# Optimization experiments

Hardware: AMD Instinct MI355X
Metric: run time of the kernel (lower is better)

## Reference

```python
import jax, jax.numpy as jnp
import numpy as np

B, G = 256, 24
N = B * G
D_IN, HEADS, D_HEAD = 128, 8, 64  # out_channels = in_channels//2 = 64, concat=False
EFF = HEADS * D_HEAD
EPS = 1e-5
SCALE = float(np.sqrt(D_HEAD))

def _gelu(x):
    return jax.nn.gelu(x, approximate=False)

def _pff(x, w1, b1, w2, b2):
    # PositionwiseFeedForward, dropout=0 (eval)
    return _gelu(x @ w1.T + b1) @ w2.T + b2

def _graph_norm_global(x, w, b, ms):
    # GraphNorm called without batch -> single graph over all N nodes
    mean = jnp.mean(x, axis=0, keepdims=True)
    out = x - mean * ms
    var = jnp.mean(out * out, axis=0, keepdims=True)
    return w * out / jnp.sqrt(var + EPS) + b

def _graph_norm(x, w, b, ms, batch, nseg):
    cnt = jax.ops.segment_sum(jnp.ones((x.shape[0],), x.dtype), batch, nseg)[:, None]
    mean = jax.ops.segment_sum(x, batch, nseg) / cnt
    out = x - mean[batch] * ms
    var = jax.ops.segment_sum(out * out, batch, nseg) / cnt
    return w * out / jnp.sqrt(var + EPS)[batch] + b

def _segment_softmax(logits, seg, nseg):
    m = jax.ops.segment_max(logits, seg, num_segments=nseg)
    e = jnp.exp(logits - m[seg])
    s = jax.ops.segment_sum(e, seg, num_segments=nseg)
    return e / (s[seg] + 1e-16)

def _attn_conv(x, edge_index, p):
    (nq_w, nq_b, nq_ms, wq, bq, wk, bk, wv, bv,
     no_w, no_b, no_ms, o_w1, o_b1, o_w2, o_b2) = p
    n = x.shape[0]
    xin = x
    xn = _graph_norm_global(x, nq_w, nq_b, nq_ms)
    q = (xn @ wq.T + bq).reshape(n, HEADS, D_HEAD)
    k = (xn @ wk.T + bk).reshape(n, HEADS, D_HEAD)
    v = (xn @ wv.T + bv).reshape(n, HEADS, D_HEAD)
    loops = jnp.arange(n, dtype=edge_index.dtype)  # add_self_loops appends
    src = jnp.concatenate([edge_index[0], loops])
    dst = jnp.concatenate([edge_index[1], loops])
    qk = jnp.sum(q[dst] * k[src], axis=-1) / SCALE          # [E', H]
    alpha = _segment_softmax(qk, dst, n)                     # segment softmax over dst
    aggr = jax.ops.segment_sum(v[src] * alpha[:, :, None], dst, num_segments=n)  # [N,H,Dh]
    aggr = aggr.mean(axis=1)                                 # concat=False: head mean -> [N,64]
    init = xin.reshape(n, D_IN // D_HEAD, D_HEAD).sum(axis=1)  # sum-fold 128 -> 64 residual
    h = aggr + init
    hn = _graph_norm_global(h, no_w, no_b, no_ms)
    return h + _pff(hn, o_w1, o_b1, o_w2, o_b2)


def setup_inputs() -> dict:
    key = jax.random.key(0)
    ks = jax.random.split(key, 12)
    # block-dense edges: fully connected within each set, no self loops
    a = np.arange(G)
    ii, jj = np.meshgrid(a, a, indexing='ij')
    m = ii != jj
    dst_l, src_l = ii[m], jj[m]
    offs = (np.arange(B) * G)[:, None]
    src = (src_l[None, :] + offs).reshape(-1)
    dst = (dst_l[None, :] + offs).reshape(-1)
    edge_index = jnp.asarray(np.stack([src, dst]), dtype=jnp.int64)
    batch = jnp.asarray(np.repeat(np.arange(B), G), dtype=jnp.int64)
    ptr = jnp.asarray(np.arange(B + 1) * G, dtype=jnp.int64)
    x = jax.random.normal(ks[0], (N, D_IN), jnp.float32)
    def lin(k, o, i):
        return jax.random.normal(k, (o, i), jnp.float32) * (1.0 / np.sqrt(i))
    d = dict(x=x, edge_index=edge_index, ptr=ptr, batch=batch)
    d.update(nq_w=jnp.ones((D_IN,)), nq_b=jnp.zeros((D_IN,)), nq_ms=jnp.ones((D_IN,)))
    d.update(wq=lin(ks[1], EFF, D_IN), bq=jnp.zeros((EFF,)),
             wk=lin(ks[2], EFF, D_IN), bk=jnp.zeros((EFF,)),
             wv=lin(ks[3], EFF, D_IN), bv=jnp.zeros((EFF,)))
    d.update(no_w=jnp.ones((D_HEAD,)), no_b=jnp.zeros((D_HEAD,)), no_ms=jnp.ones((D_HEAD,)))
    d.update(o_w1=lin(ks[4], D_HEAD, D_HEAD), o_b1=jnp.zeros((D_HEAD,)),
             o_w2=lin(ks[5], D_HEAD, D_HEAD), o_b2=jnp.zeros((D_HEAD,)))
    d.update(pn_w=jnp.ones((D_HEAD,)), pn_b=jnp.zeros((D_HEAD,)), pn_ms=jnp.ones((D_HEAD,)))
    d.update(p_w1=lin(ks[6], D_HEAD, D_HEAD), p_b1=jnp.zeros((D_HEAD,)),
             p_w2=lin(ks[7], 1, D_HEAD), p_b2=jnp.zeros((1,)))
    return d


def reference(x, edge_index, ptr, batch,
              nq_w, nq_b, nq_ms, wq, bq, wk, bk, wv, bv,
              no_w, no_b, no_ms, o_w1, o_b1, o_w2, o_b2,
              pn_w, pn_b, pn_ms, p_w1, p_b1, p_w2, p_b2):
    nseg = ptr.shape[0] - 1
    h = _attn_conv(x, edge_index,
                   (nq_w, nq_b, nq_ms, wq, bq, wk, bk, wv, bv,
                    no_w, no_b, no_ms, o_w1, o_b1, o_w2, o_b2))   # [N,64]
    hn = _graph_norm(h, pn_w, pn_b, pn_ms, batch, nseg)
    score = _pff(hn, p_w1, p_b1, p_w2, p_b2)                       # [N,1]
    w = _segment_softmax(score[:, 0], batch, nseg)[:, None]        # per-set softmax
    return jax.ops.segment_sum(x * w, batch, num_segments=nseg)    # [B, 128]
```

## Files before the change

kernel.cpp:

```cpp
#include <hip/hip_runtime.h>
#include <stdint.h>


#define N_NODES 6144
#define GSIZE 24
#define NGRAPH 256
#define DIN 128
#define DH 64
#define EFF 512
#define EPSN 1e-5f

typedef __attribute__((ext_vector_type(8))) __bf16 bf16x8;
typedef __attribute__((ext_vector_type(4))) float f32x4;
union U16B { uint4 u; bf16x8 v; unsigned short s[8]; };

__device__ inline float bf2f(unsigned short u){ return __uint_as_float(((unsigned)u)<<16); }
__device__ inline unsigned short f2bf(float f){
  unsigned u = __float_as_uint(f);
  u += 0x7fff + ((u>>16)&1);
  return (unsigned short)(u>>16);
}
__device__ inline float gelu_exact(float x){ return 0.5f*x*(1.0f+erff(x*0.70710678118654752f)); }

#define XP    0
#define HP    49152
#define WT1   81920
#define WT2   86016
#define PWT1  90112
#define FBo   94208
#define WCVT_BYTE  385024
#define HCOMB_BYTE 778240

__global__ __launch_bounds__(256)
void k_pre(const float* __restrict__ x,
           const float* __restrict__ o_w1, const float* __restrict__ o_w2,
           const float* __restrict__ p_w1,
           const float* __restrict__ o_b1, const float* __restrict__ o_b2,
           const float* __restrict__ p_b1, const float* __restrict__ p_w2,
           const float* __restrict__ p_b2,
           const float* __restrict__ wq, const float* __restrict__ wk,
           const float* __restrict__ wv,
           float* __restrict__ wsf){
  int t = threadIdx.x;
  int bi = blockIdx.x;
  if(bi < 192){
    int c = t & 127, h = t >> 7;
    float s = 0.f, q = 0.f;
    #pragma unroll
    for(int r = 0; r < 16; ++r){
      float v = x[(size_t)(bi*32 + h + 2*r)*DIN + c];
      s += v; q += v*v;
    }
    __shared__ float sm[256], sm2[256];
    sm[t] = s; sm2[t] = q;
    __syncthreads();
    if(t < 128){
      wsf[XP + bi*256 + t]       = sm[t] + sm[t+128];
      wsf[XP + bi*256 + 128 + t] = sm2[t] + sm2[t+128];
    }
    return;
  }
  if(bi < 195){
    const float* src; float* dst;
    if(bi == 192){ src = o_w1; dst = wsf + WT1; }
    else if(bi == 193){ src = o_w2; dst = wsf + WT2; }
    else { src = p_w1; dst = wsf + PWT1; }
    for(int p = t; p < DH*DH; p += 256){
      int r = p >> 6, c = p & 63;
      dst[c*DH + r] = src[p];
    }
    if(bi == 192){
      float* fb = wsf + FBo;
      if(t < 64){
        fb[t]       = o_b1[t];
        fb[64 + t]  = o_b2[t];
        fb[128 + t] = p_b1[t];
        fb[192 + t] = p_w2[t];
      }
      if(t == 0) fb[256] = p_b2[0];
    }
    return;
  }
  int j = bi - 195;
  int mat = j >> 2, seg = j & 3;
  const float* src = (mat==0) ? wq : (mat==1) ? wk : wv;
  unsigned short* dst = (unsigned short*)((char*)wsf + WCVT_BYTE)
                        + (size_t)mat*EFF*DIN + seg*16384;
  const float* sp = src + seg*16384;
  for(int e = t*8; e < 16384; e += 2048){
    float4 a = *(const float4*)(sp + e);
    float4 b = *(const float4*)(sp + e + 4);
    U16B o;
    o.s[0]=f2bf(a.x); o.s[1]=f2bf(a.y); o.s[2]=f2bf(a.z); o.s[3]=f2bf(a.w);
    o.s[4]=f2bf(b.x); o.s[5]=f2bf(b.y); o.s[6]=f2bf(b.z); o.s[7]=f2bf(b.w);
    *(uint4*)(dst + e) = o.u;
  }
}

__global__ __launch_bounds__(512, 1)
void k_fused(const float* __restrict__ x,
             const float* __restrict__ bq, const float* __restrict__ bk,
             const float* __restrict__ bv,
             const float* __restrict__ nq_w, const float* __restrict__ nq_b,
             const float* __restrict__ nq_ms,
             float* __restrict__ ws, float* __restrict__ hcomb){
  __shared__ __align__(16) char arena[52224];
  float (*hv)[68] = (float(*)[68])(arena);
  float* A1 = (float*)(arena + 6528);
  float* C1 = (float*)(arena + 7040);
  float (*qs)[GSIZE][68] = (float(*)[GSIZE][68])(arena + 7552);
  float (*ks)[GSIZE][68] = (float(*)[GSIZE][68])(arena + 20608);
  float (*vs)[GSIZE][68] = (float(*)[GSIZE][68])(arena + 33664);
  float (*S)[GSIZE][28]  = (float(*)[GSIZE][28])(arena + 46720);
  float* redA = (float*)(arena + 7552);
  float* redB = (float*)(arena + 11648);

  int t = threadIdx.x, g = blockIdx.x, base = g * GSIZE;
  const unsigned short* wcvt = (const unsigned short*)((const char*)ws + WCVT_BYTE);

  {
    int c = t & 127, grp = t >> 7;
    float s = 0.f, q = 0.f;
    for(int p = grp*48; p < grp*48 + 48; ++p){
      s += ws[XP + p*256 + c];
      q += ws[XP + p*256 + 128 + c];
    }
    redA[t] = s; redB[t] = q;
  }
  __syncthreads();
  if(t < 128){
    float s = redA[t] + redA[t+128] + redA[t+256] + redA[t+384];
    float q = redB[t] + redB[t+128] + redB[t+256] + redB[t+384];
    float mean = s * (1.0f / N_NODES);
    float ex2  = q * (1.0f / N_NODES);
    float cm   = mean * nq_ms[t];
    float var  = ex2 - 2.f*cm*mean + cm*cm;
    float rstd = rsqrtf(var + EPSN);
    float a    = nq_w[t] * rstd;
    A1[t] = a; C1[t] = nq_b[t] - a*cm;
  }
  __syncthreads();

  int pipe = t >> 8, t2 = t & 255;
  int wv4 = (t >> 6) & 3, lane = t & 63, m = lane & 15, quad = lane >> 4;
  int mt = wv4 & 1, cth = wv4 >> 1;
  int node = mt*16 + m;
  int xrow = base + node; if(xrow > N_NODES-1) xrow = N_NODES-1;

  bf16x8 xfr[4];
  #pragma unroll
  for(int kk = 0; kk < 4; kk++){
    int k0 = kk*32 + quad*8;
    float4 a = *(const float4*)(x + (size_t)xrow*DIN + k0);
    float4 b = *(const float4*)(x + (size_t)xrow*DIN + k0 + 4);
    U16B u;
    u.s[0] = f2bf(a.x*A1[k0+0] + C1[k0+0]);
    u.s[1] = f2bf(a.y*A1[k0+1] + C1[k0+1]);
    u.s[2] = f2bf(a.z*A1[k0+2] + C1[k0+2]);
    u.s[3] = f2bf(a.w*A1[k0+3] + C1[k0+3]);
    u.s[4] = f2bf(b.x*A1[k0+4] + C1[k0+4]);
    u.s[5] = f2bf(b.y*A1[k0+5] + C1[k0+5]);
    u.s[6] = f2bf(b.z*A1[k0+6] + C1[k0+6]);
    u.s[7] = f2bf(b.w*A1[k0+7] + C1[k0+7]);
    xfr[kk] = u.v;
  }

  uint4 wbuf[6][4];
  float4 bb[6];
  {
    int hh = pipe;
    #pragma unroll
    for(int task = 0; task < 6; ++task){
      int tk = cth*6 + task;
      int mat = tk >> 2, ctm = tk & 3;
      const unsigned short* wp = wcvt + (size_t)mat*EFF*DIN
                               + (size_t)(hh*64 + ctm*16 + m)*DIN + quad*8;
      #pragma unroll
      for(int kk = 0; kk < 4; kk++) wbuf[task][kk] = *(const uint4*)(wp + kk*32);
      const float* bias = (mat==0) ? bq : (mat==1) ? bk : bv;
      bb[task] = *(const float4*)(bias + hh*64 + ctm*16 + quad*4);
    }
  }

  f32x4 a0 = {0.f,0.f,0.f,0.f}, a1 = {0.f,0.f,0.f,0.f};

  for(int iter = 0; iter < 4; ++iter){
    __syncthreads();
    #pragma unroll
    for(int task = 0; task < 6; ++task){
      int tk = cth*6 + task;
      int mat = tk >> 2, ctm = tk & 3;
      f32x4 acc = {0.f,0.f,0.f,0.f};
      #pragma unroll
      for(int kk = 0; kk < 4; kk++){
        U16B w8; w8.u = wbuf[task][kk];
        acc = __builtin_amdgcn_mfma_f32_16x16x32_bf16(w8.v, xfr[kk], acc, 0, 0, 0);
      }
      float (*tile)[68] = (mat==0) ? qs[pipe] : (mat==1) ? ks[pipe] : vs[pipe];
      if(mt == 0 || m < 8){
        int d0 = ctm*16 + quad*4;
        tile[node][d0+0] = acc[0] + bb[task].x;
        tile[node][d0+1] = acc[1] + bb[task].y;
        tile[node][d0+2] = acc[2] + bb[task].z;
        tile[node][d0+3] = acc[3] + bb[task].w;
      }
    }
    __syncthreads();
    if(iter < 3){
      int hh = (iter+1)*2 + pipe;
      #pragma unroll
      for(int task = 0; task < 6; ++task){
        int tk = cth*6 + task;
        int mat = tk >> 2, ctm = tk & 3;
        const unsigned short* wp = wcvt + (size_t)mat*EFF*DIN
                                 + (size_t)(hh*64 + ctm*16 + m)*DIN + quad*8;
        #pragma unroll
        for(int kk = 0; kk < 4; kk++) wbuf[task][kk] = *(const uint4*)(wp + kk*32);
        const float* bias = (mat==0) ? bq : (mat==1) ? bk : bv;
        bb[task] = *(const float4*)(bias + hh*64 + ctm*16 + quad*4);
      }
    }
    if(t2 < 192){
      int row = t2 >> 3, sl = t2 & 7;
      const float4* qi = (const float4*)qs[pipe][row];
      const float4* k0p = (const float4*)ks[pipe][sl*3];
      const float4* k1p = (const float4*)ks[pipe][sl*3+1];
      const float4* k2p = (const float4*)ks[pipe][sl*3+2];
      float s0 = 0.f, s1 = 0.f, s2 = 0.f;
      #pragma unroll
      for(int d = 0; d < 16; ++d){
        float4 qv = qi[d];
        float4 ka = k0p[d], kb = k1p[d], kc = k2p[d];
        s0 += qv.x*ka.x + qv.y*ka.y + qv.z*ka.z + qv.w*ka.w;
        s1 += qv.x*kb.x + qv.y*kb.y + qv.z*kb.z + qv.w*kb.w;
        s2 += qv.x*kc.x + qv.y*kc.y + qv.z*kc.z + qv.w*kc.w;
      }
      s0 *= 0.125f; s1 *= 0.125f; s2 *= 0.125f;
      float m0 = fmaxf(fmaxf(s0, s1), s2);
      #pragma unroll
      for(int o = 1; o < 8; o <<= 1) m0 = fmaxf(m0, __shfl_xor(m0, o, 8));
      float e0 = __expf(s0-m0), e1 = __expf(s1-m0), e2 = __expf(s2-m0);
      float su = e0 + e1 + e2;
      #pragma unroll
      for(int o = 1; o < 8; o <<= 1) su += __shfl_xor(su, o, 8);
      float inv = 1.0f / (su + 1e-16f);
      S[pipe][row][sl*3]   = e0*inv;
      S[pipe][row][sl*3+1] = e1*inv;
      S[pipe][row][sl*3+2] = e2*inv;
    }
    __syncthreads();
    {
      int p = t2;
      if(p < 384){
        int i = p >> 4, dq = p & 15;
        #pragma unroll 8
        for(int j = 0; j < GSIZE; ++j){
          float w = S[pipe][i][j];
          float4 v = *(const float4*)&vs[pipe][j][dq*4];
          a0.x += w*v.x; a0.y += w*v.y; a0.z += w*v.z; a0.w += w*v.w;
        }
      }
      p = t2 + 256;
      if(p < 384){
        int i = p >> 4, dq = p & 15;
        #pragma unroll 8
        for(int j = 0; j < GSIZE; ++j){
          float w = S[pipe][i][j];
          float4 v = *(const float4*)&vs[pipe][j][dq*4];
          a1.x += w*v.x; a1.y += w*v.y; a1.z += w*v.z; a1.w += w*v.w;
        }
      }
    }
  }
  __syncthreads();
  if(pipe == 1){
    int p = t2;
    if(p < 384){
      int i = p >> 4, dq = p & 15;
      float4 o; o.x = a0.x*0.125f; o.y = a0.y*0.125f; o.z = a0.z*0.125f; o.w = a0.w*0.125f;
      *(float4*)&hv[i][dq*4] = o;
    }
    p = t2 + 256;
    if(p < 384){
      int i = p >> 4, dq = p & 15;
      float4 o; o.x = a1.x*0.125f; o.y = a1.y*0.125f; o.z = a1.z*0.125f; o.w = a1.w*0.125f;
      *(float4*)&hv[i][dq*4] = o;
    }
  }
  __syncthreads();
  if(pipe == 0){
    #pragma unroll
    for(int slot = 0; slot < 2; ++slot){
      int p = t2 + slot*256;
      if(p < 384){
        int i = p >> 4, dq = p & 15;
        f32x4 a = slot ? a1 : a0;
        float4 hp = *(const float4*)&hv[i][dq*4];
        const float* xr = x + (size_t)(base+i)*DIN + dq*4;
        float4 r1 = *(const float4*)xr;
        float4 r2 = *(const float4*)(xr + 64);
        float4 o;
        o.x = a.x*0.125f + hp.x + r1.x + r2.x;
        o.y = a.y*0.125f + hp.y + r1.y + r2.y;
        o.z = a.z*0.125f + hp.z + r1.z + r2.z;
        o.w = a.w*0.125f + hp.w + r1.w + r2.w;
        *(float4*)&hv[i][dq*4] = o;
        *(float4*)(hcomb + (size_t)(base+i)*DH + dq*4) = o;
      }
    }
  }
  __syncthreads();
  if(t < 64){
    float s1 = 0.f, s2 = 0.f;
    #pragma unroll
    for(int i = 0; i < GSIZE; ++i){ float v = hv[i][t]; s1 += v; s2 += v*v; }
    ws[HP + g*128 + t]      = s1;
    ws[HP + g*128 + 64 + t] = s2;
  }
}

__global__ __launch_bounds__(256)
void k_final(const float* __restrict__ x,
             const float* __restrict__ hbuf, const float* __restrict__ ws,
             const float* __restrict__ no_w, const float* __restrict__ no_b,
             const float* __restrict__ no_ms,
             const float* __restrict__ pn_w, const float* __restrict__ pn_b,
             const float* __restrict__ pn_ms,
             float* __restrict__ out){
  const float* wt1  = ws + WT1;
  const float* wt2  = ws + WT2;
  const float* pwt1 = ws + PWT1;
  const float* fb   = ws + FBo;

  __shared__ float hs[GSIZE][DH+1];
  __shared__ float hn[GSIZE][DH+1];
  __shared__ float ts[GSIZE][DH+1];
  __shared__ float A2[DH], C2[DH];
  __shared__ float a3[DH], c3[DH];
  __shared__ float scores[GSIZE], wsm[GSIZE];
  __shared__ float redA[256], redB[256];

  int t = threadIdx.x;
  int base = blockIdx.x * GSIZE;

  {
    int c = t & 63, grp = t >> 6;
    float s1 = 0.f, s2 = 0.f;
    for(int p = grp; p < NGRAPH; p += 4){
      s1 += ws[HP + p*128 + c];
      s2 += ws[HP + p*128 + 64 + c];
    }
    redA[t] = s1; redB[t] = s2;
  }
  __syncthreads();
  if(t < DH){
    float s1 = redA[t] + redA[t+64] + redA[t+128] + redA[t+192];
    float s2 = redB[t] + redB[t+64] + redB[t+128] + redB[t+192];
    float mean = s1 * (1.0f / N_NODES);
    float ex2  = s2 * (1.0f / N_NODES);
    float cm   = mean * no_ms[t];
    float var  = ex2 - 2.f*cm*mean + cm*cm;
    float rstd = rsqrtf(var + EPSN);
    float a    = no_w[t] * rstd;
    A2[t] = a; C2[t] = no_b[t] - a*cm;
  }
  __syncthreads();
  for(int p = t; p < GSIZE*DH; p += 256){
    int i = p >> 6, d = p & 63;
    float hvv = hbuf[(size_t)(base+i)*DH + d];
    hs[i][d] = hvv;
    hn[i][d] = A2[d]*hvv + C2[d];
  }
  __syncthreads();
  for(int p = t; p < GSIZE*DH; p += 256){
    int i = p >> 6, c = p & 63;
    float s = fb[c];
    #pragma unroll
    for(int k = 0; k < DH; k++) s += hn[i][k] * wt1[k*DH + c];
    ts[i][c] = gelu_exact(s);
  }
  __syncthreads();
  for(int p = t; p < GSIZE*DH; p += 256){
    int i = p >> 6, c = p & 63;
    float s = fb[64 + c];
    #pragma unroll
    for(int k = 0; k < DH; k++) s += ts[i][k] * wt2[k*DH + c];
    hs[i][c] = hs[i][c] + s;
  }
  __syncthreads();
  if(t < DH){
    float s1 = 0.f, s2 = 0.f;
    for(int i = 0; i < GSIZE; i++){ float v = hs[i][t]; s1 += v; s2 += v*v; }
    float mean = s1 * (1.0f / GSIZE);
    float ex2  = s2 * (1.0f / GSIZE);
    float cm   = mean * pn_ms[t];
    float var  = ex2 - 2.f*cm*mean + cm*cm;
    float rstd = rsqrtf(var + EPSN);
    float a    = pn_w[t] * rstd;
    a3[t] = a; c3[t] = pn_b[t] - a*cm;
  }
  __syncthreads();
  for(int p = t; p < GSIZE*DH; p += 256){
    int i = p >> 6, d = p & 63;
    hn[i][d] = a3[d]*hs[i][d] + c3[d];
  }
  __syncthreads();
  for(int p = t; p < GSIZE*DH; p += 256){
    int i = p >> 6, c = p & 63;
    float s = fb[128 + c];
    #pragma unroll
    for(int k = 0; k < DH; k++) s += hn[i][k] * pwt1[k*DH + c];
    ts[i][c] = gelu_exact(s);
  }
  __syncthreads();
  if(t < GSIZE){
    float s = fb[256];
    for(int c = 0; c < DH; c++) s += ts[t][c] * fb[192 + c];
    scores[t] = s;
  }
  __syncthreads();
  if(t < GSIZE){
    float mx = -1e30f;
    for(int j = 0; j < GSIZE; j++) mx = fmaxf(mx, scores[j]);
    float sum = 0.f;
    for(int j = 0; j < GSIZE; j++) sum += __expf(scores[j] - mx);
    wsm[t] = __expf(scores[t] - mx) / (sum + 1e-16f);
  }
  __syncthreads();
  if(t < DIN){
    float s = 0.f;
    #pragma unroll 8
    for(int i = 0; i < GSIZE; i++) s += wsm[i] * x[(size_t)(base+i)*DIN + t];
    out[(size_t)blockIdx.x*DIN + t] = s;
  }
}

extern "C" void kernel_launch(void* const* d_in, const int* in_sizes, int n_in,
                              void* d_out, int out_size, void* d_ws, size_t ws_size,
                              hipStream_t stream){
  (void)in_sizes; (void)n_in; (void)out_size; (void)ws_size;
  const float* x    = (const float*)d_in[0];
  const float* nq_w = (const float*)d_in[4];
  const float* nq_b = (const float*)d_in[5];
  const float* nq_ms= (const float*)d_in[6];
  const float* wq   = (const float*)d_in[7];
  const float* bq   = (const float*)d_in[8];
  const float* wk   = (const float*)d_in[9];
  const float* bk   = (const float*)d_in[10];
  const float* wv   = (const float*)d_in[11];
  const float* bv   = (const float*)d_in[12];
  const float* no_w = (const float*)d_in[13];
  const float* no_b = (const float*)d_in[14];
  const float* no_ms= (const float*)d_in[15];
  const float* o_w1 = (const float*)d_in[16];
  const float* o_b1 = (const float*)d_in[17];
  const float* o_w2 = (const float*)d_in[18];
  const float* o_b2 = (const float*)d_in[19];
  const float* pn_w = (const float*)d_in[20];
  const float* pn_b = (const float*)d_in[21];
  const float* pn_ms= (const float*)d_in[22];
  const float* p_w1 = (const float*)d_in[23];
  const float* p_b1 = (const float*)d_in[24];
  const float* p_w2 = (const float*)d_in[25];
  const float* p_b2 = (const float*)d_in[26];

  float* ws = (float*)d_ws;
  float* hcomb = (float*)((char*)d_ws + HCOMB_BYTE);

  k_pre<<<207, 256, 0, stream>>>(x, o_w1, o_w2, p_w1, o_b1, o_b2, p_b1, p_w2, p_b2,
                                 wq, wk, wv, ws);
  k_fused<<<NGRAPH, 512, 0, stream>>>(x, bq, bk, bv, nq_w, nq_b, nq_ms, ws, hcomb);
  k_final<<<NGRAPH, 256, 0, stream>>>(x, hcomb, ws, no_w, no_b, no_ms,
                                      pn_w, pn_b, pn_ms, (float*)d_out);
}
```

Measured before the change: 182.2 us.

## Split per-graph attention across four blocks with atomic last-block reduction

The fused attention kernel now launches 1024 blocks of 256 threads, each handling two heads of one graph, instead of 256 blocks of 512 threads handling all eight heads. Partial head sums go to a workspace buffer, and the last block per graph, found through an atomic counter, reduces them. The global-norm statistics are finalized once in the pre-kernel by a last-block pattern rather than redundantly in every block. The final kernel also stages the two 64x64 FFN weights in shared memory. The cost is an extra memset, atomics, and partial-sum traffic through global memory.

```diff
diff --git a/kernel.cpp b/kernel.cpp
--- a/kernel.cpp
+++ b/kernel.cpp
@@ -22,14 +22,18 @@
 }
 __device__ inline float gelu_exact(float x){ return 0.5f*x*(1.0f+erff(x*0.70710678118654752f)); }
 
-#define XP    0
-#define HP    49152
-#define WT1   81920
-#define WT2   86016
-#define PWT1  90112
-#define FBo   94208
-#define WCVT_BYTE  385024
-#define HCOMB_BYTE 778240
+#define XP     0
+#define A1C1   49152
+#define HP     49408
+#define WT1    82176
+#define WT2    86272
+#define PWT1   90368
+#define FBo    94464
+#define XPCNT  95232
+#define CNT    95233
+#define WCVT_BYTE  382976
+#define HPART_BYTE 776192
+#define HCOMB_BYTE 7067648
 
 __global__ __launch_bounds__(256)
 void k_pre(const float* __restrict__ x,
@@ -40,6 +44,8 @@
            const float* __restrict__ p_b2,
            const float* __restrict__ wq, const float* __restrict__ wk,
            const float* __restrict__ wv,
+           const float* __restrict__ nq_w, const float* __restrict__ nq_b,
+           const float* __restrict__ nq_ms,
            float* __restrict__ wsf){
   int t = threadIdx.x;
   int bi = blockIdx.x;
@@ -52,11 +58,35 @@
       s += v; q += v*v;
     }
     __shared__ float sm[256], sm2[256];
+    __shared__ int lastf;
     sm[t] = s; sm2[t] = q;
     __syncthreads();
     if(t < 128){
       wsf[XP + bi*256 + t]       = sm[t] + sm[t+128];
       wsf[XP + bi*256 + 128 + t] = sm2[t] + sm2[t+128];
+    }
+    __syncthreads();
+    if(t == 0){
+      __threadfence();
+      int old = atomicAdd((int*)(wsf + XPCNT), 1);
+      lastf = (old == 191);
+    }
+    __syncthreads();
+    if(!lastf) return;
+    __threadfence();
+    float acc = 0.f;
+    for(int p = 0; p < 192; ++p) acc += wsf[XP + p*256 + t];
+    sm[t] = acc;
+    __syncthreads();
+    if(t < 128){
+      float mean = sm[t] * (1.0f / N_NODES);
+      float ex2  = sm[128+t] * (1.0f / N_NODES);
+      float cm   = mean * nq_ms[t];
+      float var  = ex2 - 2.f*cm*mean + cm*cm;
+      float rstd = rsqrtf(var + EPSN);
+      float a    = nq_w[t] * rstd;
+      wsf[A1C1 + t]       = a;
+      wsf[A1C1 + 128 + t] = nq_b[t] - a*cm;
     }
     return;
   }
@@ -97,78 +127,52 @@
   }
 }
 
-__global__ __launch_bounds__(512, 1)
+__global__ __launch_bounds__(256, 4)
 void k_fused(const float* __restrict__ x,
              const float* __restrict__ bq, const float* __restrict__ bk,
              const float* __restrict__ bv,
-             const float* __restrict__ nq_w, const float* __restrict__ nq_b,
-             const float* __restrict__ nq_ms,
              float* __restrict__ ws, float* __restrict__ hcomb){
-  __shared__ __align__(16) char arena[52224];
-  float (*hv)[68] = (float(*)[68])(arena);
-  float* A1 = (float*)(arena + 6528);
-  float* C1 = (float*)(arena + 7040);
-  float (*qs)[GSIZE][68] = (float(*)[GSIZE][68])(arena + 7552);
-  float (*ks)[GSIZE][68] = (float(*)[GSIZE][68])(arena + 20608);
-  float (*vs)[GSIZE][68] = (float(*)[GSIZE][68])(arena + 33664);
-  float (*S)[GSIZE][28]  = (float(*)[GSIZE][28])(arena + 46720);
-  float* redA = (float*)(arena + 7552);
-  float* redB = (float*)(arena + 11648);
-
-  int t = threadIdx.x, g = blockIdx.x, base = g * GSIZE;
+  __shared__ __align__(16) float hv[GSIZE][68];
+  __shared__ float A1s[128], C1s[128];
+  __shared__ __align__(16) float qs[GSIZE][68], ks[GSIZE][68], vs[GSIZE][68];
+  __shared__ __align__(16) float S[GSIZE][28];
+  __shared__ int lastf;
+
+  int t = threadIdx.x, b = blockIdx.x;
+  int g = b >> 2, quarter = b & 3, base = g * GSIZE;
   const unsigned short* wcvt = (const unsigned short*)((const char*)ws + WCVT_BYTE);
-
-  {
-    int c = t & 127, grp = t >> 7;
-    float s = 0.f, q = 0.f;
-    for(int p = grp*48; p < grp*48 + 48; ++p){
-      s += ws[XP + p*256 + c];
-      q += ws[XP + p*256 + 128 + c];
-    }
-    redA[t] = s; redB[t] = q;
-  }
-  __syncthreads();
-  if(t < 128){
-    float s = redA[t] + redA[t+128] + redA[t+256] + redA[t+384];
-    float q = redB[t] + redB[t+128] + redB[t+256] + redB[t+384];
-    float mean = s * (1.0f / N_NODES);
-    float ex2  = q * (1.0f / N_NODES);
-    float cm   = mean * nq_ms[t];
-    float var  = ex2 - 2.f*cm*mean + cm*cm;
-    float rstd = rsqrtf(var + EPSN);
-    float a    = nq_w[t] * rstd;
-    A1[t] = a; C1[t] = nq_b[t] - a*cm;
-  }
-  __syncthreads();
-
-  int pipe = t >> 8, t2 = t & 255;
-  int wv4 = (t >> 6) & 3, lane = t & 63, m = lane & 15, quad = lane >> 4;
+  float* hpart = (float*)((char*)ws + HPART_BYTE);
+
+  if(t < 128){ A1s[t] = ws[A1C1 + t]; C1s[t] = ws[A1C1 + 128 + t]; }
+  __syncthreads();
+
+  int wv4 = t >> 6, lane = t & 63, m = lane & 15, quad = lane >> 4;
   int mt = wv4 & 1, cth = wv4 >> 1;
   int node = mt*16 + m;
-  int xrow = base + node; if(xrow > N_NODES-1) xrow = N_NODES-1;
+  int xrow = base + ((node < GSIZE) ? node : 0);
 
   bf16x8 xfr[4];
   #pragma unroll
   for(int kk = 0; kk < 4; kk++){
     int k0 = kk*32 + quad*8;
     float4 a = *(const float4*)(x + (size_t)xrow*DIN + k0);
-    float4 b = *(const float4*)(x + (size_t)xrow*DIN + k0 + 4);
+    float4 bfl = *(const float4*)(x + (size_t)xrow*DIN + k0 + 4);
     U16B u;
-    u.s[0] = f2bf(a.x*A1[k0+0] + C1[k0+0]);
-    u.s[1] = f2bf(a.y*A1[k0+1] + C1[k0+1]);
-    u.s[2] = f2bf(a.z*A1[k0+2] + C1[k0+2]);
-    u.s[3] = f2bf(a.w*A1[k0+3] + C1[k0+3]);
-    u.s[4] = f2bf(b.x*A1[k0+4] + C1[k0+4]);
-    u.s[5] = f2bf(b.y*A1[k0+5] + C1[k0+5]);
-    u.s[6] = f2bf(b.z*A1[k0+6] + C1[k0+6]);
-    u.s[7] = f2bf(b.w*A1[k0+7] + C1[k0+7]);
+    u.s[0] = f2bf(a.x*A1s[k0+0] + C1s[k0+0]);
+    u.s[1] = f2bf(a.y*A1s[k0+1] + C1s[k0+1]);
+    u.s[2] = f2bf(a.z*A1s[k0+2] + C1s[k0+2]);
+    u.s[3] = f2bf(a.w*A1s[k0+3] + C1s[k0+3]);
+    u.s[4] = f2bf(bfl.x*A1s[k0+4] + C1s[k0+4]);
+    u.s[5] = f2bf(bfl.y*A1s[k0+5] + C1s[k0+5]);
+    u.s[6] = f2bf(bfl.z*A1s[k0+6] + C1s[k0+6]);
+    u.s[7] = f2bf(bfl.w*A1s[k0+7] + C1s[k0+7]);
     xfr[kk] = u.v;
   }
 
   uint4 wbuf[6][4];
   float4 bb[6];
   {
-    int hh = pipe;
+    int hh = quarter*2;
     #pragma unroll
     for(int task = 0; task < 6; ++task){
       int tk = cth*6 + task;
@@ -184,7 +188,7 @@
 
   f32x4 a0 = {0.f,0.f,0.f,0.f}, a1 = {0.f,0.f,0.f,0.f};
 
-  for(int iter = 0; iter < 4; ++iter){
+  for(int iter = 0; iter < 2; ++iter){
     __syncthreads();
     #pragma unroll
     for(int task = 0; task < 6; ++task){
@@ -196,7 +200,7 @@
         U16B w8; w8.u = wbuf[task][kk];
         acc = __builtin_amdgcn_mfma_f32_16x16x32_bf16(w8.v, xfr[kk], acc, 0, 0, 0);
       }
-      float (*tile)[68] = (mat==0) ? qs[pipe] : (mat==1) ? ks[pipe] : vs[pipe];
+      float (*tile)[68] = (mat==0) ? qs : (mat==1) ? ks : vs;
       if(mt == 0 || m < 8){
         int d0 = ctm*16 + quad*4;
         tile[node][d0+0] = acc[0] + bb[task].x;
@@ -206,8 +210,8 @@
       }
     }
     __syncthreads();
-    if(iter < 3){
-      int hh = (iter+1)*2 + pipe;
+    if(iter == 0){
+      int hh = quarter*2 + 1;
       #pragma unroll
       for(int task = 0; task < 6; ++task){
         int tk = cth*6 + task;
@@ -220,12 +224,12 @@
         bb[task] = *(const float4*)(bias + hh*64 + ctm*16 + quad*4);
       }
     }
-    if(t2 < 192){
-      int row = t2 >> 3, sl = t2 & 7;
-      const float4* qi = (const float4*)qs[pipe][row];
-      const float4* k0p = (const float4*)ks[pipe][sl*3];
-      const float4* k1p = (const float4*)ks[pipe][sl*3+1];
-      const float4* k2p = (const float4*)ks[pipe][sl*3+2];
+    if(t < 192){
+      int row = t >> 3, sl = t & 7;
+      const float4* qi = (const float4*)qs[row];
+      const float4* k0p = (const float4*)ks[sl*3];
+      const float4* k1p = (const float4*)ks[sl*3+1];
+      const float4* k2p = (const float4*)ks[sl*3+2];
       float s0 = 0.f, s1 = 0.f, s2 = 0.f;
       #pragma unroll
       for(int d = 0; d < 16; ++d){
@@ -244,69 +248,87 @@
       #pragma unroll
       for(int o = 1; o < 8; o <<= 1) su += __shfl_xor(su, o, 8);
       float inv = 1.0f / (su + 1e-16f);
-      S[pipe][row][sl*3]   = e0*inv;
-      S[pipe][row][sl*3+1] = e1*inv;
-      S[pipe][row][sl*3+2] = e2*inv;
+      S[row][sl*3]   = e0*inv;
+      S[row][sl*3+1] = e1*inv;
+      S[row][sl*3+2] = e2*inv;
     }
     __syncthreads();
     {
-      int p = t2;
-      if(p < 384){
-        int i = p >> 4, dq = p & 15;
+      int i = t >> 4, dq = t & 15;
+      #pragma unroll 8
+      for(int j = 0; j < GSIZE; ++j){
+        float w = S[i][j];
+        float4 v = *(const float4*)&vs[j][dq*4];
+        a0.x += w*v.x; a0.y += w*v.y; a0.z += w*v.z; a0.w += w*v.w;
+      }
+      if(t < 128){
+        int p = t + 256; int i2 = p >> 4, dq2 = p & 15;
         #pragma unroll 8
         for(int j = 0; j < GSIZE; ++j){
-          float w = S[pipe][i][j];
-          float4 v = *(const float4*)&vs[pipe][j][dq*4];
-          a0.x += w*v.x; a0.y += w*v.y; a0.z += w*v.z; a0.w += w*v.w;
-        }
-      }
-      p = t2 + 256;
-      if(p < 384){
-        int i = p >> 4, dq = p & 15;
-        #pragma unroll 8
-        for(int j = 0; j < GSIZE; ++j){
-          float w = S[pipe][i][j];
-          float4 v = *(const float4*)&vs[pipe][j][dq*4];
+          float w = S[i2][j];
+          float4 v = *(const float4*)&vs[j][dq2*4];
           a1.x += w*v.x; a1.y += w*v.y; a1.z += w*v.z; a1.w += w*v.w;
         }
       }
     }
   }
   __syncthreads();
-  if(pipe == 1){
-    int p = t2;
-    if(p < 384){
-      int i = p >> 4, dq = p & 15;
-      float4 o; o.x = a0.x*0.125f; o.y = a0.y*0.125f; o.z = a0.z*0.125f; o.w = a0.w*0.125f;
-      *(float4*)&hv[i][dq*4] = o;
-    }
-    p = t2 + 256;
-    if(p < 384){
-      int i = p >> 4, dq = p & 15;
-      float4 o; o.x = a1.x*0.125f; o.y = a1.y*0.125f; o.z = a1.z*0.125f; o.w = a1.w*0.125f;
-      *(float4*)&hv[i][dq*4] = o;
-    }
-  }
-  __syncthreads();
-  if(pipe == 0){
-    #pragma unroll
-    for(int slot = 0; slot < 2; ++slot){
-      int p = t2 + slot*256;
-      if(p < 384){
-        int i = p >> 4, dq = p & 15;
-        f32x4 a = slot ? a1 : a0;
-        float4 hp = *(const float4*)&hv[i][dq*4];
-        const float* xr = x + (size_t)(base+i)*DIN + dq*4;
+  {
+    int i = t >> 4, dq = t & 15;
+    float4 o; o.x = a0.x*0.125f; o.y = a0.y*0.125f; o.z = a0.z*0.125f; o.w = a0.w*0.125f;
+    if(quarter == 0){
+      const float* xr = x + (size_t)(base+i)*DIN + dq*4;
+      float4 r1 = *(const float4*)xr;
+      float4 r2 = *(const float4*)(xr + 64);
+      o.x += r1.x + r2.x; o.y += r1.y + r2.y; o.z += r1.z + r2.z; o.w += r1.w + r2.w;
+    }
+    *(float4*)&hv[i][dq*4] = o;
+    *(float4*)(hpart + ((size_t)b*GSIZE + i)*DH + dq*4) = o;
+    if(t < 128){
+      int p = t + 256; int i2 = p >> 4, dq2 = p & 15;
+      float4 o2; o2.x = a1.x*0.125f; o2.y = a1.y*0.125f; o2.z = a1.z*0.125f; o2.w = a1.w*0.125f;
+      if(quarter == 0){
+        const float* xr = x + (size_t)(base+i2)*DIN + dq2*4;
         float4 r1 = *(const float4*)xr;
         float4 r2 = *(const float4*)(xr + 64);
-        float4 o;
-        o.x = a.x*0.125f + hp.x + r1.x + r2.x;
-        o.y = a.y*0.125f + hp.y + r1.y + r2.y;
-        o.z = a.z*0.125f + hp.z + r1.z + r2.z;
-        o.w = a.w*0.125f + hp.w + r1.w + r2.w;
-        *(float4*)&hv[i][dq*4] = o;
-        *(float4*)(hcomb + (size_t)(base+i)*DH + dq*4) = o;
-      }
+        o2.x += r1.x + r2.x; o2.y += r1.y + r2.y; o2.z += r1.z + r2.z; o2.w += r1.w + r2.w;
+      }
+      *(float4*)&hv[i2][dq2*4] = o2;
+      *(float4*)(hpart + ((size_t)b*GSIZE + i2)*DH + dq2*4) = o2;
+    }
+  }
+  __syncthreads();
+  if(t == 0){
+    __threadfence();
+    int old = atomicAdd((int*)(ws + CNT) + g, 1);
+    lastf = (old == 3);
+  }
+  __syncthreads();
+  if(!lastf) return;
+  __threadfence();
+  {
+    int gb = g << 2;
+    int i = t >> 4, dq = t & 15;
+    float4 o = *(float4*)&hv[i][dq*4];
+    #pragma unroll
+    for(int qq = 0; qq < 4; ++qq){
+      if(qq == quarter) continue;
+      float4 pv = *(const float4*)(hpart + ((size_t)(gb+qq)*GSIZE + i)*DH + dq*4);
+      o.x += pv.x; o.y += pv.y; o.z += pv.z; o.w += pv.w;
+    }
+    *(float4*)&hv[i][dq*4] = o;
+    *(float4*)(hcomb + (size_t)(base+i)*DH + dq*4) = o;
+    if(t < 128){
+      int p = t + 256; int i2 = p >> 4, dq2 = p & 15;
+      float4 o2 = *(float4*)&hv[i2][dq2*4];
+      #pragma unroll
+      for(int qq = 0; qq < 4; ++qq){
+        if(qq == quarter) continue;
+        float4 pv = *(const float4*)(hpart + ((size_t)(gb+qq)*GSIZE + i2)*DH + dq2*4);
+        o2.x += pv.x; o2.y += pv.y; o2.z += pv.z; o2.w += pv.w;
+      }
+      *(float4*)&hv[i2][dq2*4] = o2;
+      *(float4*)(hcomb + (size_t)(base+i2)*DH + dq2*4) = o2;
     }
   }
   __syncthreads();
@@ -327,14 +349,13 @@
              const float* __restrict__ pn_w, const float* __restrict__ pn_b,
              const float* __restrict__ pn_ms,
              float* __restrict__ out){
-  const float* wt1  = ws + WT1;
-  const float* wt2  = ws + WT2;
   const float* pwt1 = ws + PWT1;
   const float* fb   = ws + FBo;
 
-  __shared__ float hs[GSIZE][DH+1];
-  __shared__ float hn[GSIZE][DH+1];
-  __shared__ float ts[GSIZE][DH+1];
+  __shared__ float wt1s[64][64], wt2s[64][64];
+  __shared__ float hs[GSIZE][DH];
+  __shared__ float hn[GSIZE][DH];
+  __shared__ float ts[GSIZE][DH];
   __shared__ float A2[DH], C2[DH];
   __shared__ float a3[DH], c3[DH];
   __shared__ float scores[GSIZE], wsm[GSIZE];
@@ -343,6 +364,10 @@
   int t = threadIdx.x;
   int base = blockIdx.x * GSIZE;
 
+  for(int p = t; p < DH*DH; p += 256){
+    wt1s[p>>6][p&63] = ws[WT1 + p];
+    wt2s[p>>6][p&63] = ws[WT2 + p];
+  }
   {
     int c = t & 63, grp = t >> 6;
     float s1 = 0.f, s2 = 0.f;
@@ -376,7 +401,7 @@
     int i = p >> 6, c = p & 63;
     float s = fb[c];
     #pragma unroll
-    for(int k = 0; k < DH; k++) s += hn[i][k] * wt1[k*DH + c];
+    for(int k = 0; k < DH; k++) s += hn[i][k] * wt1s[k][c];
     ts[i][c] = gelu_exact(s);
   }
   __syncthreads();
@@ -384,7 +409,7 @@
     int i = p >> 6, c = p & 63;
     float s = fb[64 + c];
     #pragma unroll
-    for(int k = 0; k < DH; k++) s += ts[i][k] * wt2[k*DH + c];
+    for(int k = 0; k < DH; k++) s += ts[i][k] * wt2s[k][c];
     hs[i][c] = hs[i][c] + s;
   }
   __syncthreads();
@@ -467,9 +492,10 @@
   float* ws = (float*)d_ws;
   float* hcomb = (float*)((char*)d_ws + HCOMB_BYTE);
 
+  hipMemsetAsync((char*)d_ws + (size_t)XPCNT*4, 0, 1028, stream);
   k_pre<<<207, 256, 0, stream>>>(x, o_w1, o_w2, p_w1, o_b1, o_b2, p_b1, p_w2, p_b2,
-                                 wq, wk, wv, ws);
-  k_fused<<<NGRAPH, 512, 0, stream>>>(x, bq, bk, bv, nq_w, nq_b, nq_ms, ws, hcomb);
+                                 wq, wk, wv, nq_w, nq_b, nq_ms, ws);
+  k_fused<<<1024, 256, 0, stream>>>(x, bq, bk, bv, ws, hcomb);
   k_final<<<NGRAPH, 256, 0, stream>>>(x, hcomb, ws, no_w, no_b, no_ms,
                                       pn_w, pn_b, pn_ms, (float*)d_out);
 }
```

After: 297.0 us. +62.9%, slower.

## Compute input GraphNorm coefficients once in last k_pre block; stage FFN weights in LDS

Applied to the files above, without the earlier changes.

Previously every k_fused block re-reduced all 192 partial column sums to derive the input GraphNorm scale and shift, which is redundant global traffic across 256 blocks. Now the last-arriving k_pre block, detected with an atomic counter and threadfence, computes those coefficients once and stores them in the workspace. k_fused just loads them. k_final also caches the two 64x64 PFF weight matrices in shared memory instead of reading them from global memory in the inner loop. The cost is an extra memset launch to reset the counter, a serialized tail reduction in k_pre, and relaxed launch bounds plus a changed workspace layout.

```diff
diff --git a/kernel.cpp b/kernel.cpp
--- a/kernel.cpp
+++ b/kernel.cpp
@@ -22,14 +22,16 @@
 }
 __device__ inline float gelu_exact(float x){ return 0.5f*x*(1.0f+erff(x*0.70710678118654752f)); }
 
-#define XP    0
-#define HP    49152
-#define WT1   81920
-#define WT2   86016
-#define PWT1  90112
-#define FBo   94208
-#define WCVT_BYTE  385024
-#define HCOMB_BYTE 778240
+#define XP     0
+#define A1C1   49152
+#define HP     49408
+#define WT1    82176
+#define WT2    86272
+#define PWT1   90368
+#define FBo    94464
+#define XPCNT  95232
+#define WCVT_BYTE  382976
+#define HCOMB_BYTE 7067648
 
 __global__ __launch_bounds__(256)
 void k_pre(const float* __restrict__ x,
@@ -40,6 +42,8 @@
            const float* __restrict__ p_b2,
            const float* __restrict__ wq, const float* __restrict__ wk,
            const float* __restrict__ wv,
+           const float* __restrict__ nq_w, const float* __restrict__ nq_b,
+           const float* __restrict__ nq_ms,
            float* __restrict__ wsf){
   int t = threadIdx.x;
   int bi = blockIdx.x;
@@ -52,11 +56,35 @@
       s += v; q += v*v;
     }
     __shared__ float sm[256], sm2[256];
+    __shared__ int lastf;
     sm[t] = s; sm2[t] = q;
     __syncthreads();
     if(t < 128){
       wsf[XP + bi*256 + t]       = sm[t] + sm[t+128];
       wsf[XP + bi*256 + 128 + t] = sm2[t] + sm2[t+128];
+    }
+    __syncthreads();
+    if(t == 0){
+      __threadfence();
+      int old = atomicAdd((int*)(wsf + XPCNT), 1);
+      lastf = (old == 191);
+    }
+    __syncthreads();
+    if(!lastf) return;
+    __threadfence();
+    float acc = 0.f;
+    for(int p = 0; p < 192; ++p) acc += wsf[XP + p*256 + t];
+    sm[t] = acc;
+    __syncthreads();
+    if(t < 128){
+      float mean = sm[t] * (1.0f / N_NODES);
+      float ex2  = sm[128+t] * (1.0f / N_NODES);
+      float cm   = mean * nq_ms[t];
+      float var  = ex2 - 2.f*cm*mean + cm*cm;
+      float rstd = rsqrtf(var + EPSN);
+      float a    = nq_w[t] * rstd;
+      wsf[A1C1 + t]       = a;
+      wsf[A1C1 + 128 + t] = nq_b[t] - a*cm;
     }
     return;
   }
@@ -97,71 +125,43 @@
   }
 }
 
-__global__ __launch_bounds__(512, 1)
+__global__ __launch_bounds__(512)
 void k_fused(const float* __restrict__ x,
              const float* __restrict__ bq, const float* __restrict__ bk,
              const float* __restrict__ bv,
-             const float* __restrict__ nq_w, const float* __restrict__ nq_b,
-             const float* __restrict__ nq_ms,
              float* __restrict__ ws, float* __restrict__ hcomb){
-  __shared__ __align__(16) char arena[52224];
-  float (*hv)[68] = (float(*)[68])(arena);
-  float* A1 = (float*)(arena + 6528);
-  float* C1 = (float*)(arena + 7040);
-  float (*qs)[GSIZE][68] = (float(*)[GSIZE][68])(arena + 7552);
-  float (*ks)[GSIZE][68] = (float(*)[GSIZE][68])(arena + 20608);
-  float (*vs)[GSIZE][68] = (float(*)[GSIZE][68])(arena + 33664);
-  float (*S)[GSIZE][28]  = (float(*)[GSIZE][28])(arena + 46720);
-  float* redA = (float*)(arena + 7552);
-  float* redB = (float*)(arena + 11648);
+  __shared__ __align__(16) float hv[GSIZE][68];
+  __shared__ float A1s[128], C1s[128];
+  __shared__ __align__(16) float qs[2][GSIZE][68], ks[2][GSIZE][68], vs[2][GSIZE][68];
+  __shared__ __align__(16) float S[2][GSIZE][28];
 
   int t = threadIdx.x, g = blockIdx.x, base = g * GSIZE;
   const unsigned short* wcvt = (const unsigned short*)((const char*)ws + WCVT_BYTE);
 
-  {
-    int c = t & 127, grp = t >> 7;
-    float s = 0.f, q = 0.f;
-    for(int p = grp*48; p < grp*48 + 48; ++p){
-      s += ws[XP + p*256 + c];
-      q += ws[XP + p*256 + 128 + c];
-    }
-    redA[t] = s; redB[t] = q;
-  }
-  __syncthreads();
-  if(t < 128){
-    float s = redA[t] + redA[t+128] + redA[t+256] + redA[t+384];
-    float q = redB[t] + redB[t+128] + redB[t+256] + redB[t+384];
-    float mean = s * (1.0f / N_NODES);
-    float ex2  = q * (1.0f / N_NODES);
-    float cm   = mean * nq_ms[t];
-    float var  = ex2 - 2.f*cm*mean + cm*cm;
-    float rstd = rsqrtf(var + EPSN);
-    float a    = nq_w[t] * rstd;
-    A1[t] = a; C1[t] = nq_b[t] - a*cm;
-  }
+  if(t < 128){ A1s[t] = ws[A1C1 + t]; C1s[t] = ws[A1C1 + 128 + t]; }
   __syncthreads();
 
   int pipe = t >> 8, t2 = t & 255;
   int wv4 = (t >> 6) & 3, lane = t & 63, m = lane & 15, quad = lane >> 4;
   int mt = wv4 & 1, cth = wv4 >> 1;
   int node = mt*16 + m;
-  int xrow = base + node; if(xrow > N_NODES-1) xrow = N_NODES-1;
+  int xrow = base + ((node < GSIZE) ? node : 0);
 
   bf16x8 xfr[4];
   #pragma unroll
   for(int kk = 0; kk < 4; kk++){
     int k0 = kk*32 + quad*8;
     float4 a = *(const float4*)(x + (size_t)xrow*DIN + k0);
-    float4 b = *(const float4*)(x + (size_t)xrow*DIN + k0 + 4);
+    float4 bfl = *(const float4*)(x + (size_t)xrow*DIN + k0 + 4);
     U16B u;
-    u.s[0] = f2bf(a.x*A1[k0+0] + C1[k0+0]);
-    u.s[1] = f2bf(a.y*A1[k0+1] + C1[k0+1]);
-    u.s[2] = f2bf(a.z*A1[k0+2] + C1[k0+2]);
-    u.s[3] = f2bf(a.w*A1[k0+3] + C1[k0+3]);
-    u.s[4] = f2bf(b.x*A1[k0+4] + C1[k0+4]);
-    u.s[5] = f2bf(b.y*A1[k0+5] + C1[k0+5]);
-    u.s[6] = f2bf(b.z*A1[k0+6] + C1[k0+6]);
-    u.s[7] = f2bf(b.w*A1[k0+7] + C1[k0+7]);
+    u.s[0] = f2bf(a.x*A1s[k0+0] + C1s[k0+0]);
+    u.s[1] = f2bf(a.y*A1s[k0+1] + C1s[k0+1]);
+    u.s[2] = f2bf(a.z*A1s[k0+2] + C1s[k0+2]);
+    u.s[3] = f2bf(a.w*A1s[k0+3] + C1s[k0+3]);
+    u.s[4] = f2bf(bfl.x*A1s[k0+4] + C1s[k0+4]);
+    u.s[5] = f2bf(bfl.y*A1s[k0+5] + C1s[k0+5]);
+    u.s[6] = f2bf(bfl.z*A1s[k0+6] + C1s[k0+6]);
+    u.s[7] = f2bf(bfl.w*A1s[k0+7] + C1s[k0+7]);
     xfr[kk] = u.v;
   }
 
@@ -327,14 +327,13 @@
              const float* __restrict__ pn_w, const float* __restrict__ pn_b,
              const float* __restrict__ pn_ms,
              float* __restrict__ out){
-  const float* wt1  = ws + WT1;
-  const float* wt2  = ws + WT2;
   const float* pwt1 = ws + PWT1;
   const float* fb   = ws + FBo;
 
-  __shared__ float hs[GSIZE][DH+1];
-  __shared__ float hn[GSIZE][DH+1];
-  __shared__ float ts[GSIZE][DH+1];
+  __shared__ float wt1s[64][64], wt2s[64][64];
+  __shared__ float hs[GSIZE][DH];
+  __shared__ float hn[GSIZE][DH];
+  __shared__ float ts[GSIZE][DH];
   __shared__ float A2[DH], C2[DH];
   __shared__ float a3[DH], c3[DH];
   __shared__ float scores[GSIZE], wsm[GSIZE];
@@ -343,6 +342,10 @@
   int t = threadIdx.x;
   int base = blockIdx.x * GSIZE;
 
+  for(int p = t; p < DH*DH; p += 256){
+    wt1s[p>>6][p&63] = ws[WT1 + p];
+    wt2s[p>>6][p&63] = ws[WT2 + p];
+  }
   {
     int c = t & 63, grp = t >> 6;
     float s1 = 0.f, s2 = 0.f;
@@ -376,7 +379,7 @@
     int i = p >> 6, c = p & 63;
     float s = fb[c];
     #pragma unroll
-    for(int k = 0; k < DH; k++) s += hn[i][k] * wt1[k*DH + c];
+    for(int k = 0; k < DH; k++) s += hn[i][k] * wt1s[k][c];
     ts[i][c] = gelu_exact(s);
   }
   __syncthreads();
@@ -384,7 +387,7 @@
     int i = p >> 6, c = p & 63;
     float s = fb[64 + c];
     #pragma unroll
-    for(int k = 0; k < DH; k++) s += ts[i][k] * wt2[k*DH + c];
+    for(int k = 0; k < DH; k++) s += ts[i][k] * wt2s[k][c];
     hs[i][c] = hs[i][c] + s;
   }
   __syncthreads();
@@ -467,9 +470,10 @@
   float* ws = (float*)d_ws;
   float* hcomb = (float*)((char*)d_ws + HCOMB_BYTE);
 
+  hipMemsetAsync((char*)d_ws + (size_t)XPCNT*4, 0, 4, stream);
   k_pre<<<207, 256, 0, stream>>>(x, o_w1, o_w2, p_w1, o_b1, o_b2, p_b1, p_w2, p_b2,
-                                 wq, wk, wv, ws);
-  k_fused<<<NGRAPH, 512, 0, stream>>>(x, bq, bk, bv, nq_w, nq_b, nq_ms, ws, hcomb);
+                                 wq, wk, wv, nq_w, nq_b, nq_ms, ws);
+  k_fused<<<NGRAPH, 512, 0, stream>>>(x, bq, bk, bv, ws, hcomb);
   k_final<<<NGRAPH, 256, 0, stream>>>(x, hcomb, ws, no_w, no_b, no_ms,
                                       pn_w, pn_b, pn_ms, (float*)d_out);
 }
```

New measurement: 187.3 us. 1.03x slower.
